# Optimization experiments

Measured on AMD Instinct MI355X. Metric: run time of the kernel, lower is better.

Reference implementation:

```python
import jax, jax.numpy as jnp
import numpy as np
import math

B, S, DIM, H = 4, 1024, 4096, 32
HD = DIM // H  # head_dim = 128
MAX_B, MAX_S = 4, 1024
START_POS = 0
ROPE_THETA = 10000.0


def setup_inputs() -> dict:
    key = jax.random.key(0)
    ks = jax.random.split(key, 6)
    x = jax.random.normal(ks[0], (B, S, DIM), dtype=jnp.float32)
    # real RoPE frequencies: freqs_cis[t, j] = exp(i * t * theta^{-2j/hd})
    inv_freq = 1.0 / (ROPE_THETA ** (jnp.arange(0, HD, 2, dtype=jnp.float32) / HD))  # [HD/2]
    t = jnp.arange(START_POS, START_POS + S, dtype=jnp.float32)
    ang = jnp.outer(t, inv_freq)  # [S, HD/2]
    freqs_cos = jnp.cos(ang)
    freqs_sin = jnp.sin(ang)
    # additive causal mask as in llama: -inf above diagonal offset start_pos+1
    mask = jnp.triu(jnp.full((1, 1, S, S), float('-inf'), dtype=jnp.float32), k=START_POS + 1)
    scale = 0.02
    wq = jax.random.normal(ks[1], (DIM, DIM), dtype=jnp.float32) * scale
    wk = jax.random.normal(ks[2], (DIM, DIM), dtype=jnp.float32) * scale
    wv = jax.random.normal(ks[3], (DIM, DIM), dtype=jnp.float32) * scale
    wo = jax.random.normal(ks[4], (DIM, DIM), dtype=jnp.float32) * scale
    cache_k = jnp.zeros((MAX_B, MAX_S, H, HD), dtype=jnp.float32)
    cache_v = jnp.zeros((MAX_B, MAX_S, H, HD), dtype=jnp.float32)
    return {"x": x, "start_pos": START_POS, "freqs_cos": freqs_cos, "freqs_sin": freqs_sin,
            "mask": mask, "wq": wq, "wk": wk, "wv": wv, "wo": wo,
            "cache_k": cache_k, "cache_v": cache_v}


def _apply_rotary(t, cos, sin):
    # t: [B, S, H, HD]; interpret last dim as HD/2 complex pairs (real, imag)
    b, s, h, d = t.shape
    tr = t.reshape(b, s, h, d // 2, 2)
    a, bb = tr[..., 0], tr[..., 1]
    c = cos[None, :, None, :]  # [1, S, 1, HD/2]
    si = sin[None, :, None, :]
    out_r = a * c - bb * si
    out_i = a * si + bb * c
    return jnp.stack([out_r, out_i], axis=-1).reshape(b, s, h, d)


def reference(x, start_pos, freqs_cos, freqs_sin, mask, wq, wk, wv, wo, cache_k, cache_v):
    bsz, seqlen, dim = x.shape
    hd = HD
    # torch Linear: y = x @ W.T, W is [out, in]
    xq = (x @ wq.T).reshape(bsz, seqlen, H, hd)
    xk = (x @ wk.T).reshape(bsz, seqlen, H, hd)
    xv = (x @ wv.T).reshape(bsz, seqlen, H, hd)
    xq = _apply_rotary(xq, freqs_cos, freqs_sin)
    xk = _apply_rotary(xk, freqs_cos, freqs_sin)
    # KV-cache write
    cache_k = jax.lax.dynamic_update_slice(cache_k, xk, (0, start_pos, 0, 0))
    cache_v = jax.lax.dynamic_update_slice(cache_v, xv, (0, start_pos, 0, 0))
    keys = cache_k[:bsz, :start_pos + seqlen]    # [B, K, H, HD]
    values = cache_v[:bsz, :start_pos + seqlen]  # [B, K, H, HD]
    # naive attention: full score matrix
    scores = jnp.einsum('bqhd,bkhd->bhqk', xq, keys) / math.sqrt(hd)
    scores = scores + mask
    probs = jax.nn.softmax(scores.astype(jnp.float32), axis=-1).astype(xq.dtype)
    out = jnp.einsum('bhqk,bkhd->bqhd', probs, values)
    out = out.reshape(bsz, seqlen, -1)
    return out @ wo.T
```

## Files before the change

### kernel.cpp

```cpp
#include <hip/hip_runtime.h>
#include <hip/hip_bf16.h>
#include <cstdint>

typedef __hip_bfloat16 bf16;
typedef __attribute__((ext_vector_type(8))) short frag8;
typedef __attribute__((ext_vector_type(4))) float f32x4;

#define DEV __device__ __forceinline__

DEV void gl_lds16(const void* g, void* l) {
  __builtin_amdgcn_global_load_lds(
      (const __attribute__((address_space(1))) void*)g,
      (__attribute__((address_space(3))) void*)l, 16, 0, 0);
}

DEV void storeC(float* C, size_t idx, float v) { C[idx] = v; }
DEV void storeC(bf16* C, size_t idx, float v) { C[idx] = __float2bfloat16(v); }

__global__ __launch_bounds__(256) void conv_kernel(const float* __restrict__ in,
                                                   bf16* __restrict__ out, int n8) {
  int i = blockIdx.x * 256 + threadIdx.x;
  if (i >= n8) return;
  const float4* in4 = reinterpret_cast<const float4*>(in);
  float4 a = in4[2 * i], b = in4[2 * i + 1];
  union { frag8 v; bf16 h[8]; } u;
  u.h[0] = __float2bfloat16(a.x); u.h[1] = __float2bfloat16(a.y);
  u.h[2] = __float2bfloat16(a.z); u.h[3] = __float2bfloat16(a.w);
  u.h[4] = __float2bfloat16(b.x); u.h[5] = __float2bfloat16(b.y);
  u.h[6] = __float2bfloat16(b.z); u.h[7] = __float2bfloat16(b.w);
  *reinterpret_cast<frag8*>(out + (size_t)i * 8) = u.v;
}

#define MF(a, b, c) __builtin_amdgcn_mfma_f32_16x16x32_bf16(a, b, c, 0, 0, 0)

#define STAGE(isB, h, tt, bp) do {                                             \
    char* _d = lds + ((isB) * 65536) + ((((bp) * 2) + (h)) << 14);             \
    gl_lds16(((isB) ? gB : gA)[h][0] + (size_t)(tt) * 64, _d + ldsOff0);       \
    gl_lds16(((isB) ? gB : gA)[h][1] + (size_t)(tt) * 64, _d + ldsOff1);       \
  } while (0)

#define RDA(mi, ckk) (*(const frag8*)(ab + aRowB + (mi) * 2048 + (ckk)))
#define RDB(ni, ckk) (*(const frag8*)(bb + bRowB + (ni) * 2048 + (ckk)))

#define PHASE(p, SSTAGE, SWAIT) do {                                           \
    if ((p) == 0) {                                                            \
      b00 = RDB(0, ck0); b01 = RDB(0, ck1); b10 = RDB(1, ck0); b11 = RDB(1, ck1); \
      b20 = RDB(2, ck0); b21 = RDB(2, ck1); b30 = RDB(3, ck0); b31 = RDB(3, ck1); \
    }                                                                          \
    frag8 a00 = RDA(2 * (p), ck0), a01 = RDA(2 * (p), ck1);                    \
    frag8 a10 = RDA(2 * (p) + 1, ck0), a11 = RDA(2 * (p) + 1, ck1);            \
    SSTAGE;                                                                    \
    SWAIT;                                                                     \
    __builtin_amdgcn_s_barrier();                                              \
    __builtin_amdgcn_s_setprio(1);                                             \
    acc[2*(p)][0]   = MF(a00, b00, acc[2*(p)][0]);                             \
    acc[2*(p)][1]   = MF(a00, b10, acc[2*(p)][1]);                             \
    acc[2*(p)][2]   = MF(a00, b20, acc[2*(p)][2]);                             \
    acc[2*(p)][3]   = MF(a00, b30, acc[2*(p)][3]);                             \
    acc[2*(p)+1][0] = MF(a10, b00, acc[2*(p)+1][0]);                           \
    acc[2*(p)+1][1] = MF(a10, b10, acc[2*(p)+1][1]);                           \
    acc[2*(p)+1][2] = MF(a10, b20, acc[2*(p)+1][2]);                           \
    acc[2*(p)+1][3] = MF(a10, b30, acc[2*(p)+1][3]);                           \
    acc[2*(p)][0]   = MF(a01, b01, acc[2*(p)][0]);                             \
    acc[2*(p)][1]   = MF(a01, b11, acc[2*(p)][1]);                             \
    acc[2*(p)][2]   = MF(a01, b21, acc[2*(p)][2]);                             \
    acc[2*(p)][3]   = MF(a01, b31, acc[2*(p)][3]);                             \
    acc[2*(p)+1][0] = MF(a11, b01, acc[2*(p)+1][0]);                           \
    acc[2*(p)+1][1] = MF(a11, b11, acc[2*(p)+1][1]);                           \
    acc[2*(p)+1][2] = MF(a11, b21, acc[2*(p)+1][2]);                           \
    acc[2*(p)+1][3] = MF(a11, b31, acc[2*(p)+1][3]);                           \
    __builtin_amdgcn_s_setprio(0);                                             \
    __builtin_amdgcn_s_barrier();                                              \
  } while (0)

#define VM4 asm volatile("s_waitcnt vmcnt(4)" ::: "memory")
#define VM0 asm volatile("s_waitcnt vmcnt(0)" ::: "memory")
#define NOW ((void)0)

#define TILE(t, SA, SB, SWAIT) do {                                            \
    const int _bp2 = ((t) & 1) * 2;                                            \
    char* ab = lds + ((_bp2 + wm) << 14);                                      \
    char* bb = lds + 65536 + ((_bp2 + bhalf) << 14);                           \
    PHASE(0, { if (SA) STAGE(0, 0, (t) + 1, ((t) + 1) & 1); }, NOW);           \
    PHASE(1, { if (SA) STAGE(0, 1, (t) + 1, ((t) + 1) & 1); }, NOW);           \
    PHASE(2, { if (SB) STAGE(1, 0, (t) + 2, (t) & 1); }, NOW);                 \
    PHASE(3, { if (SB) STAGE(1, 1, (t) + 2, (t) & 1); }, SWAIT);               \
  } while (0)

template <typename OutT>
__global__ __launch_bounds__(512, 2) void gemm8(const bf16* __restrict__ A,
                                                const bf16* __restrict__ Bt,
                                                OutT* __restrict__ C) {
  __shared__ __align__(16) char lds[131072];
  const int K = 4096, N = 4096;
  const int t = threadIdx.x;
  const int lane = t & 63, w = t >> 6;
  const int wm = w >> 2, wn = w & 3;
  const int lr = lane & 15, lg = lane >> 4;
  const int bhalf = wn >> 1;

  const int bid = blockIdx.x;
  const int wg = (bid & 7) * 32 + (bid >> 3);
  const int m0 = (wg >> 4) * 256, n0 = (wg & 15) * 256;

  const bf16* gA[2][2];
  const bf16* gB[2][2];
  int ldsOff0, ldsOff1;
  {
    int c0 = (w * 2 + 0) * 64 + lane;
    int c1 = (w * 2 + 1) * 64 + lane;
    int r0 = c0 >> 3, r1 = c1 >> 3;
    int e0 = ((c0 & 7) ^ (r0 & 7)) * 8;
    int e1 = ((c1 & 7) ^ (r1 & 7)) * 8;
    ldsOff0 = c0 * 16; ldsOff1 = c1 * 16;
    gA[0][0] = A + (size_t)(m0 + r0) * K + e0;
    gA[0][1] = A + (size_t)(m0 + r1) * K + e1;
    gA[1][0] = A + (size_t)(m0 + 128 + r0) * K + e0;
    gA[1][1] = A + (size_t)(m0 + 128 + r1) * K + e1;
    gB[0][0] = Bt + (size_t)(n0 + r0) * K + e0;
    gB[0][1] = Bt + (size_t)(n0 + r1) * K + e1;
    gB[1][0] = Bt + (size_t)(n0 + 128 + r0) * K + e0;
    gB[1][1] = Bt + (size_t)(n0 + 128 + r1) * K + e1;
  }

  const int swz = (lr & 7) << 4;
  const int ck0 = (lg * 16) ^ swz;
  const int ck1 = (64 + lg * 16) ^ swz;
  const int aRowB = lr * 128;
  const int bRowB = ((wn & 1) * 64 + lr) * 128;

  f32x4 acc[8][4];
#pragma unroll
  for (int mi = 0; mi < 8; ++mi)
#pragma unroll
    for (int ni = 0; ni < 4; ++ni) acc[mi][ni] = (f32x4){0.f, 0.f, 0.f, 0.f};

  frag8 b00, b01, b10, b11, b20, b21, b30, b31;

  STAGE(1, 0, 0, 0); STAGE(1, 1, 0, 0);
  STAGE(0, 0, 0, 0); STAGE(0, 1, 0, 0);
  STAGE(1, 0, 1, 1); STAGE(1, 1, 1, 1);
  VM4;
  __builtin_amdgcn_s_barrier();

  for (int tt = 0; tt < 62; tt += 2) {
    TILE(tt, 1, 1, VM4);
    TILE(tt + 1, 1, 1, VM4);
  }
  TILE(62, 1, 0, VM0);
  TILE(63, 0, 0, NOW);

#pragma unroll
  for (int mi = 0; mi < 8; ++mi)
#pragma unroll
    for (int ni = 0; ni < 4; ++ni) {
      f32x4 v = acc[mi][ni];
      int col = n0 + wn * 64 + ni * 16 + lr;
#pragma unroll
      for (int i = 0; i < 4; ++i) {
        int row = m0 + wm * 128 + mi * 16 + lg * 4 + i;
        storeC(C, (size_t)row * N + col, v[i]);
      }
    }
}

__global__ __launch_bounds__(256) void rope_kernel(bf16* __restrict__ q, bf16* __restrict__ k,
                                                   const float* __restrict__ fc,
                                                   const float* __restrict__ fs) {
  int idx = blockIdx.x * 256 + threadIdx.x;
  int i = idx & 63;
  int s = (idx >> 11) & 1023;
  float c = fc[s * 64 + i], sn = fs[s * 64 + i];
  uint32_t* qp = reinterpret_cast<uint32_t*>(q) + idx;
  uint32_t* kp = reinterpret_cast<uint32_t*>(k) + idx;
  union { uint32_t u; bf16 h[2]; } a, r;
  a.u = *qp;
  {
    float x = __bfloat162float(a.h[0]), y = __bfloat162float(a.h[1]);
    r.h[0] = __float2bfloat16(x * c - y * sn);
    r.h[1] = __float2bfloat16(x * sn + y * c);
    *qp = r.u;
  }
  a.u = *kp;
  {
    float x = __bfloat162float(a.h[0]), y = __bfloat162float(a.h[1]);
    r.h[0] = __float2bfloat16(x * c - y * sn);
    r.h[1] = __float2bfloat16(x * sn + y * c);
    *kp = r.u;
  }
}

__global__ __launch_bounds__(256) void transpose_v_kernel(const bf16* __restrict__ v,
                                                          bf16* __restrict__ vt) {
  __shared__ unsigned short tile[32][40];
  const int st = blockIdx.x * 32;
  const int dt = blockIdx.y * 32;
  const int bh = blockIdx.z;
  const int b = bh >> 5, h = bh & 31;
  const int t = threadIdx.x;
  const int r = t >> 3, c4 = (t & 7) * 4;
  const unsigned short* src = reinterpret_cast<const unsigned short*>(v) +
      ((size_t)(b * 1024 + st + r)) * 4096 + h * 128 + dt + c4;
  uint2 d = *reinterpret_cast<const uint2*>(src);
  tile[r][c4 + 0] = (unsigned short)(d.x & 0xffff);
  tile[r][c4 + 1] = (unsigned short)(d.x >> 16);
  tile[r][c4 + 2] = (unsigned short)(d.y & 0xffff);
  tile[r][c4 + 3] = (unsigned short)(d.y >> 16);
  __syncthreads();
  uint2 o;
  o.x = (uint32_t)tile[c4 + 0][r] | ((uint32_t)tile[c4 + 1][r] << 16);
  o.y = (uint32_t)tile[c4 + 2][r] | ((uint32_t)tile[c4 + 3][r] << 16);
  unsigned short* dst = reinterpret_cast<unsigned short*>(vt) +
      ((size_t)bh * 128 + dt + r) * 1024 + st + c4;
  *reinterpret_cast<uint2*>(dst) = o;
}

__global__ __launch_bounds__(512, 4) void attn_kernel(const bf16* __restrict__ q,
                                                      const bf16* __restrict__ k,
                                                      const bf16* __restrict__ vt,
                                                      bf16* __restrict__ out) {
  __shared__ __align__(16) char als[81920];
  const int qt = blockIdx.x, h = blockIdx.y, b = blockIdx.z;
  const int t = threadIdx.x;
  const int lane = t & 63, w = t >> 6;
  const int lr = lane & 15, lg = lane >> 4;
  const int NT = 2 * qt + 2;

  frag8 aq[4];
  {
    const bf16* qp = q + ((size_t)(b * 1024 + qt * 128 + w * 16 + lr)) * 4096 + h * 128 + lg * 8;
#pragma unroll
    for (int ks = 0; ks < 4; ++ks) aq[ks] = *reinterpret_cast<const frag8*>(qp + ks * 32);
  }

  const bf16* kbase = k + (size_t)b * 1024 * 4096 + h * 128;
  const bf16* vbase = vt + ((size_t)(b * 32 + h)) * 128 * 1024;

  const int L0 = t * 16, L1 = (t + 512) * 16;
  const int kr0 = L0 >> 8, kr1 = L1 >> 8;
  const size_t kOff0 = (size_t)kr0 * 4096 + (((L0 & 255) ^ ((kr0 & 7) << 4)) >> 1);
  const size_t kOff1 = (size_t)kr1 * 4096 + (((L1 & 255) ^ ((kr1 & 7) << 4)) >> 1);
  const int vr0 = L0 >> 7, vr1 = L1 >> 7;
  const size_t vOff0 = (size_t)vr0 * 1024 + (((L0 & 127) ^ ((vr0 & 7) << 4)) >> 1);
  const size_t vOff1 = (size_t)vr1 * 1024 + (((L1 & 127) ^ ((vr1 & 7) << 4)) >> 1);

#define STAGE_K(tt, bp) do { char* _d = als + (bp) * 16384;                    \
    gl_lds16(kbase + (size_t)(tt) * 262144 + kOff0, _d + L0);                  \
    gl_lds16(kbase + (size_t)(tt) * 262144 + kOff1, _d + L1); } while (0)
#define STAGE_V(tt, bp) do { char* _d = als + 32768 + (bp) * 16384;            \
    gl_lds16(vbase + (size_t)(tt) * 64 + vOff0, _d + L0);                      \
    gl_lds16(vbase + (size_t)(tt) * 64 + vOff1, _d + L1); } while (0)

  f32x4 oacc[8] = {};
  float mrow = -1e30f, lrow = 0.f;
  char* Pw = als + 65536 + w * 2048;
  const float scale = 0.08838834764831845f;
  const int qmaxw = qt * 128 + w * 16 + 15;
  const int qr_g = qt * 128 + w * 16 + lr;

  STAGE_K(0, 0); STAGE_V(0, 0);
  STAGE_K(1, 1); STAGE_V(1, 1);

  for (int kt = 0; kt < NT; ++kt) {
    const int cur = kt & 1;
    const bool act = (kt * 64 <= qmaxw);
    const bool domask = (kt >= 2 * qt);
    char* Kc = als + cur * 16384;
    char* Vc = als + 32768 + cur * 16384;

    if (kt + 1 < NT) { VM4; } else { VM0; }
    __builtin_amdgcn_s_barrier();

    f32x4 sacc[4] = {};
    if (act) {
      __builtin_amdgcn_s_setprio(1);
#pragma unroll
      for (int ks = 0; ks < 4; ++ks) {
#pragma unroll
        for (int ni = 0; ni < 4; ++ni) {
          int n = ni * 16 + lr;
          frag8 bk = *reinterpret_cast<const frag8*>(
              Kc + n * 256 + ((ks * 64 + lg * 16) ^ ((n & 7) << 4)));
          sacc[ni] = MF(bk, aq[ks], sacc[ni]);
        }
      }
      __builtin_amdgcn_s_setprio(0);
    }
    __builtin_amdgcn_s_barrier();
    if (kt + 2 < NT) STAGE_K(kt + 2, cur);

    if (act) {
#pragma unroll
      for (int ni = 0; ni < 4; ++ni)
#pragma unroll
        for (int i = 0; i < 4; ++i) {
          float x = sacc[ni][i] * scale;
          if (domask) {
            int kc = kt * 64 + ni * 16 + lg * 4 + i;
            if (kc > qr_g) x = -1e30f;
          }
          sacc[ni][i] = x;
        }

      float pm = sacc[0][0];
#pragma unroll
      for (int ni = 0; ni < 4; ++ni)
#pragma unroll
        for (int i = 0; i < 4; ++i) pm = fmaxf(pm, sacc[ni][i]);
      pm = fmaxf(pm, __shfl_xor(pm, 16));
      pm = fmaxf(pm, __shfl_xor(pm, 32));
      float mn = fmaxf(mrow, pm);
      float f = __expf(mrow - mn);
      float rs = 0.f;
#pragma unroll
      for (int ni = 0; ni < 4; ++ni)
#pragma unroll
        for (int i = 0; i < 4; ++i) {
          float p = __expf(sacc[ni][i] - mn);
          sacc[ni][i] = p;
          rs += p;
        }
      rs += __shfl_xor(rs, 16);
      rs += __shfl_xor(rs, 32);
      lrow = lrow * f + rs;
      mrow = mn;

#pragma unroll
      for (int ni = 0; ni < 4; ++ni)
#pragma unroll
        for (int j = 0; j < 2; ++j) {
          union { uint32_t u; bf16 hh[2]; } pk;
          pk.hh[0] = __float2bfloat16(sacc[ni][2 * j]);
          pk.hh[1] = __float2bfloat16(sacc[ni][2 * j + 1]);
          int kc2 = (ni * 16 + lg * 4 + 2 * j) * 2;
          *reinterpret_cast<uint32_t*>(Pw + lr * 128 + (kc2 ^ ((lr & 7) << 4))) = pk.u;
        }

      float fi0 = __shfl(f, lg * 4 + 0);
      float fi1 = __shfl(f, lg * 4 + 1);
      float fi2 = __shfl(f, lg * 4 + 2);
      float fi3 = __shfl(f, lg * 4 + 3);
#pragma unroll
      for (int nj = 0; nj < 8; ++nj) {
        oacc[nj][0] *= fi0; oacc[nj][1] *= fi1;
        oacc[nj][2] *= fi2; oacc[nj][3] *= fi3;
      }

      __builtin_amdgcn_s_setprio(1);
#pragma unroll
      for (int ks2 = 0; ks2 < 2; ++ks2) {
        frag8 ap = *reinterpret_cast<const frag8*>(
            Pw + lr * 128 + ((ks2 * 64 + lg * 16) ^ ((lr & 7) << 4)));
#pragma unroll
        for (int nj = 0; nj < 8; ++nj) {
          int d = nj * 16 + lr;
          frag8 bv = *reinterpret_cast<const frag8*>(
              Vc + d * 128 + ((ks2 * 64 + lg * 16) ^ ((d & 7) << 4)));
          oacc[nj] = MF(ap, bv, oacc[nj]);
        }
      }
      __builtin_amdgcn_s_setprio(0);
    }
    __builtin_amdgcn_s_barrier();
    if (kt + 2 < NT) STAGE_V(kt + 2, cur);
  }

  float lv0 = __shfl(lrow, lg * 4 + 0);
  float lv1 = __shfl(lrow, lg * 4 + 1);
  float lv2 = __shfl(lrow, lg * 4 + 2);
  float lv3 = __shfl(lrow, lg * 4 + 3);
#pragma unroll
  for (int nj = 0; nj < 8; ++nj) {
    int srow0 = qt * 128 + w * 16 + lg * 4;
    size_t base = ((size_t)(b * 1024 + srow0)) * 4096 + h * 128 + nj * 16 + lr;
    out[base]          = __float2bfloat16(oacc[nj][0] / lv0);
    out[base + 4096]   = __float2bfloat16(oacc[nj][1] / lv1);
    out[base + 8192]   = __float2bfloat16(oacc[nj][2] / lv2);
    out[base + 12288]  = __float2bfloat16(oacc[nj][3] / lv3);
  }
#undef STAGE_K
#undef STAGE_V
}

extern "C" void kernel_launch(void* const* d_in, const int* in_sizes, int n_in,
                              void* d_out, int out_size, void* d_ws, size_t ws_size,
                              hipStream_t stream) {
  const float* x  = (const float*)d_in[0];
  const float* fc = (const float*)d_in[2];
  const float* fs = (const float*)d_in[3];
  const float* wq = (const float*)d_in[5];
  const float* wk = (const float*)d_in[6];
  const float* wv = (const float*)d_in[7];
  const float* wo = (const float*)d_in[8];
  float* out = (float*)d_out;

  const size_t SZ = (size_t)4096 * 4096 * 2;
  char* w = (char*)d_ws;
  bf16* xb = (bf16*)(w);
  bf16* wb = (bf16*)(w + SZ);
  bf16* qb = (bf16*)(w + 2 * SZ);
  bf16* kb = (bf16*)(w + 3 * SZ);
  bf16* vb = (bf16*)(w + 4 * SZ);
  bf16* vtb = xb;
  bf16* ao  = vb;

  const int n8 = 4096 * 4096 / 8;
  dim3 cgrd(n8 / 256), blk(256);
  dim3 ggrd(256);
  dim3 gblk(512);

  conv_kernel<<<cgrd, blk, 0, stream>>>(x, xb, n8);
  conv_kernel<<<cgrd, blk, 0, stream>>>(wq, wb, n8);
  gemm8<bf16><<<ggrd, gblk, 0, stream>>>(xb, wb, qb);
  conv_kernel<<<cgrd, blk, 0, stream>>>(wk, wb, n8);
  gemm8<bf16><<<ggrd, gblk, 0, stream>>>(xb, wb, kb);
  conv_kernel<<<cgrd, blk, 0, stream>>>(wv, wb, n8);
  gemm8<bf16><<<ggrd, gblk, 0, stream>>>(xb, wb, vb);
  rope_kernel<<<dim3(32768), blk, 0, stream>>>(qb, kb, fc, fs);
  transpose_v_kernel<<<dim3(32, 4, 128), blk, 0, stream>>>(vb, vtb);
  attn_kernel<<<dim3(8, 32, 4), gblk, 0, stream>>>(qb, kb, vtb, ao);
  conv_kernel<<<cgrd, blk, 0, stream>>>(wo, wb, n8);
  gemm8<float><<<ggrd, gblk, 0, stream>>>(ao, wb, out);
}
```

Before: 686.1 us.

## Fuse RoPE into projection GEMM epilogue and pass P via shuffles in attention

Applies the rotary embedding inside the Q and K GEMM epilogue, using a lane-pair shuffle to get each element's partner, and drops the separate rope kernel with its extra read and write of Q and K. In the attention kernel, the softmax probabilities are no longer staged through an LDS scratch buffer. They are repacked into the MFMA A-operand layout with cross-lane shuffles, which cuts LDS use from 80 KB to 64 KB per block. The cost is extra epilogue work and global loads of cos and sin tables in the GEMM, plus more shuffle instructions in the attention inner loop.

Result: no change. 677.3 us (-1.3%).

```diff
diff --git a/kernel.cpp b/kernel.cpp
--- a/kernel.cpp
+++ b/kernel.cpp
@@ -87,10 +87,12 @@
     PHASE(3, { if (SB) STAGE(1, 1, (t) + 2, (t) & 1); }, SWAIT);               \
   } while (0)
 
-template <typename OutT>
+template <typename OutT, bool ROPE>
 __global__ __launch_bounds__(512, 2) void gemm8(const bf16* __restrict__ A,
                                                 const bf16* __restrict__ Bt,
-                                                OutT* __restrict__ C) {
+                                                OutT* __restrict__ C,
+                                                const float* __restrict__ fc,
+                                                const float* __restrict__ fs) {
   __shared__ __align__(16) char lds[131072];
   const int K = 4096, N = 4096;
   const int t = threadIdx.x;
@@ -156,38 +158,27 @@
     for (int ni = 0; ni < 4; ++ni) {
       f32x4 v = acc[mi][ni];
       int col = n0 + wn * 64 + ni * 16 + lr;
-#pragma unroll
-      for (int i = 0; i < 4; ++i) {
-        int row = m0 + wm * 128 + mi * 16 + lg * 4 + i;
-        storeC(C, (size_t)row * N + col, v[i]);
+      if (ROPE) {
+        int i = (col & 127) >> 1;
+        const bool odd = (col & 1);
+#pragma unroll
+        for (int ii = 0; ii < 4; ++ii) {
+          int row = m0 + wm * 128 + mi * 16 + lg * 4 + ii;
+          int s = row & 1023;
+          float c = fc[s * 64 + i], si = fs[s * 64 + i];
+          float val = v[ii];
+          float par = __shfl_xor(val, 1);
+          float o = val * c + (odd ? par * si : -par * si);
+          storeC(C, (size_t)row * N + col, o);
+        }
+      } else {
+#pragma unroll
+        for (int ii = 0; ii < 4; ++ii) {
+          int row = m0 + wm * 128 + mi * 16 + lg * 4 + ii;
+          storeC(C, (size_t)row * N + col, v[ii]);
+        }
       }
     }
-}
-
-__global__ __launch_bounds__(256) void rope_kernel(bf16* __restrict__ q, bf16* __restrict__ k,
-                                                   const float* __restrict__ fc,
-                                                   const float* __restrict__ fs) {
-  int idx = blockIdx.x * 256 + threadIdx.x;
-  int i = idx & 63;
-  int s = (idx >> 11) & 1023;
-  float c = fc[s * 64 + i], sn = fs[s * 64 + i];
-  uint32_t* qp = reinterpret_cast<uint32_t*>(q) + idx;
-  uint32_t* kp = reinterpret_cast<uint32_t*>(k) + idx;
-  union { uint32_t u; bf16 h[2]; } a, r;
-  a.u = *qp;
-  {
-    float x = __bfloat162float(a.h[0]), y = __bfloat162float(a.h[1]);
-    r.h[0] = __float2bfloat16(x * c - y * sn);
-    r.h[1] = __float2bfloat16(x * sn + y * c);
-    *qp = r.u;
-  }
-  a.u = *kp;
-  {
-    float x = __bfloat162float(a.h[0]), y = __bfloat162float(a.h[1]);
-    r.h[0] = __float2bfloat16(x * c - y * sn);
-    r.h[1] = __float2bfloat16(x * sn + y * c);
-    *kp = r.u;
-  }
 }
 
 __global__ __launch_bounds__(256) void transpose_v_kernel(const bf16* __restrict__ v,
@@ -219,7 +210,7 @@
                                                       const bf16* __restrict__ k,
                                                       const bf16* __restrict__ vt,
                                                       bf16* __restrict__ out) {
-  __shared__ __align__(16) char als[81920];
+  __shared__ __align__(16) char als[65536];
   const int qt = blockIdx.x, h = blockIdx.y, b = blockIdx.z;
   const int t = threadIdx.x;
   const int lane = t & 63, w = t >> 6;
@@ -253,7 +244,6 @@
 
   f32x4 oacc[8] = {};
   float mrow = -1e30f, lrow = 0.f;
-  char* Pw = als + 65536 + w * 2048;
   const float scale = 0.08838834764831845f;
   const int qmaxw = qt * 128 + w * 16 + 15;
   const int qr_g = qt * 128 + w * 16 + lr;
@@ -325,15 +315,15 @@
       lrow = lrow * f + rs;
       mrow = mn;
 
+      uint32_t Wrd[8];
 #pragma unroll
       for (int ni = 0; ni < 4; ++ni)
 #pragma unroll
-        for (int j = 0; j < 2; ++j) {
+        for (int jj = 0; jj < 2; ++jj) {
           union { uint32_t u; bf16 hh[2]; } pk;
-          pk.hh[0] = __float2bfloat16(sacc[ni][2 * j]);
-          pk.hh[1] = __float2bfloat16(sacc[ni][2 * j + 1]);
-          int kc2 = (ni * 16 + lg * 4 + 2 * j) * 2;
-          *reinterpret_cast<uint32_t*>(Pw + lr * 128 + (kc2 ^ ((lr & 7) << 4))) = pk.u;
+          pk.hh[0] = __float2bfloat16(sacc[ni][2 * jj]);
+          pk.hh[1] = __float2bfloat16(sacc[ni][2 * jj + 1]);
+          Wrd[ni * 2 + jj] = pk.u;
         }
 
       float fi0 = __shfl(f, lg * 4 + 0);
@@ -349,14 +339,20 @@
       __builtin_amdgcn_s_setprio(1);
 #pragma unroll
       for (int ks2 = 0; ks2 < 2; ++ks2) {
-        frag8 ap = *reinterpret_cast<const frag8*>(
-            Pw + lr * 128 + ((ks2 * 64 + lg * 16) ^ ((lr & 7) << 4)));
+        union { frag8 fr; uint32_t w[4]; } apu;
+#pragma unroll
+        for (int j2 = 0; j2 < 4; ++j2) {
+          int src = lr + (((2 * lg) + (j2 >> 1)) & 3) * 16;
+          uint32_t lo = __shfl(Wrd[4 * ks2 + (j2 & 1)], src);
+          uint32_t hi = __shfl(Wrd[4 * ks2 + 2 + (j2 & 1)], src);
+          apu.w[j2] = (lg & 2) ? hi : lo;
+        }
 #pragma unroll
         for (int nj = 0; nj < 8; ++nj) {
           int d = nj * 16 + lr;
           frag8 bv = *reinterpret_cast<const frag8*>(
               Vc + d * 128 + ((ks2 * 64 + lg * 16) ^ ((d & 7) << 4)));
-          oacc[nj] = MF(ap, bv, oacc[nj]);
+          oacc[nj] = MF(apu.fr, bv, oacc[nj]);
         }
       }
       __builtin_amdgcn_s_setprio(0);
@@ -411,14 +407,13 @@
 
   conv_kernel<<<cgrd, blk, 0, stream>>>(x, xb, n8);
   conv_kernel<<<cgrd, blk, 0, stream>>>(wq, wb, n8);
-  gemm8<bf16><<<ggrd, gblk, 0, stream>>>(xb, wb, qb);
+  gemm8<bf16, true><<<ggrd, gblk, 0, stream>>>(xb, wb, qb, fc, fs);
   conv_kernel<<<cgrd, blk, 0, stream>>>(wk, wb, n8);
-  gemm8<bf16><<<ggrd, gblk, 0, stream>>>(xb, wb, kb);
+  gemm8<bf16, true><<<ggrd, gblk, 0, stream>>>(xb, wb, kb, fc, fs);
   conv_kernel<<<cgrd, blk, 0, stream>>>(wv, wb, n8);
-  gemm8<bf16><<<ggrd, gblk, 0, stream>>>(xb, wb, vb);
-  rope_kernel<<<dim3(32768), blk, 0, stream>>>(qb, kb, fc, fs);
+  gemm8<bf16, false><<<ggrd, gblk, 0, stream>>>(xb, wb, vb, fc, fs);
   transpose_v_kernel<<<dim3(32, 4, 128), blk, 0, stream>>>(vb, vtb);
   attn_kernel<<<dim3(8, 32, 4), gblk, 0, stream>>>(qb, kb, vtb, ao);
   conv_kernel<<<cgrd, blk, 0, stream>>>(wo, wb, n8);
-  gemm8<float><<<ggrd, gblk, 0, stream>>>(ao, wb, out);
-}
+  gemm8<float, false><<<ggrd, gblk, 0, stream>>>(ao, wb, out, fc, fs);
+}
```
